# Kernel optimization log

Measured on AMD Instinct MI355X. Metric: run time of the kernel, lower is better.

## Reference

```python
import jax, jax.numpy as jnp
import numpy as np

FEAT_DIM = 128
MAX_ATOMS = 15
MAX_AA = 22
MAX_RELPOS = 32
NUM_FUNCS = 3
BB_N, BB_CA, BB_C = 0, 1, 2  # backbone heavy-atom indices


def setup_inputs() -> dict:
    key = jax.random.key(0)
    ks = jax.random.split(key, 12)
    N, L, A, D = 2, 256, MAX_ATOMS, FEAT_DIM
    s = 0.02
    aa = jax.random.randint(ks[0], (N, L), 0, MAX_AA)
    res_nb = jnp.sort(jax.random.randint(ks[1], (N, L), 0, 500), axis=1)
    chain_nb = jax.random.randint(ks[2], (N, L), 0, 2)
    pos_atoms = jax.random.normal(ks[3], (N, L, A, 3), dtype=jnp.float32) * 3.0
    mask_atoms = jnp.ones((N, L, A), dtype=jnp.float32)
    dihed_dim = 2 * (1 + 4 * NUM_FUNCS)  # 26
    return dict(
        aa=aa, res_nb=res_nb, chain_nb=chain_nb,
        pos_atoms=pos_atoms, mask_atoms=mask_atoms,
        aa_embed_w=jax.random.normal(ks[4], (MAX_AA * MAX_AA, D), jnp.float32) * s,
        relpos_embed_w=jax.random.normal(ks[5], (2 * MAX_RELPOS + 1, D), jnp.float32) * s,
        distcoef_w=jnp.zeros((MAX_AA * MAX_AA, A * A), jnp.float32),  # Constant(0.0) init
        dist_w1=jax.random.normal(ks[6], (A * A, D), jnp.float32) * s,
        dist_b1=jnp.zeros((D,), jnp.float32),
        dist_w2=jax.random.normal(ks[7], (D, D), jnp.float32) * s,
        dist_b2=jnp.zeros((D,), jnp.float32),
        out_w1=jax.random.normal(ks[8], (3 * D + dihed_dim, D), jnp.float32) * s,
        out_b1=jnp.zeros((D,), jnp.float32),
        out_w2=jax.random.normal(ks[9], (D, D), jnp.float32) * s,
        out_b2=jnp.zeros((D,), jnp.float32),
        out_w3=jax.random.normal(ks[10], (D, D), jnp.float32) * s,
        out_b3=jnp.zeros((D,), jnp.float32),
    )


def _dihedral(p0, p1, p2, p3, eps=1e-10):
    # dihedral angle from four points, broadcasting over leading dims
    v0 = p2 - p1
    v1 = p0 - p1
    v2 = p3 - p2
    u1 = jnp.cross(v0, v1)
    u2 = jnp.cross(v0, v2)
    n1 = u1 / jnp.sqrt(jnp.sum(u1 * u1, -1, keepdims=True) + eps)
    n2 = u2 / jnp.sqrt(jnp.sum(u2 * u2, -1, keepdims=True) + eps)
    sgn = jnp.sign(jnp.sum(jnp.cross(v0, n1) * n2, -1))
    cosang = jnp.clip(jnp.sum(n1 * n2, -1), -1.0 + 1e-7, 1.0 - 1e-7)
    return jnp.nan_to_num(sgn * jnp.arccos(cosang))


def _angular_encoding(x):
    # freq bands [1,2,3, 1,1/2,1/3] (num_funcs=3); out dim = d*(1+4*num_funcs)
    freqs = jnp.asarray([1.0, 2.0, 3.0, 1.0, 0.5, 1.0 / 3.0], dtype=x.dtype)
    xe = x[..., None]
    code = jnp.concatenate([xe, jnp.sin(xe * freqs), jnp.cos(xe * freqs)], axis=-1)
    return code.reshape(x.shape[:-1] + (-1,))


def reference(aa, res_nb, chain_nb, pos_atoms, mask_atoms,
              aa_embed_w, relpos_embed_w, distcoef_w,
              dist_w1, dist_b1, dist_w2, dist_b2,
              out_w1, out_b1, out_w2, out_b2, out_w3, out_b3):
    N, L = aa.shape
    A = mask_atoms.shape[-1]

    mask_res = mask_atoms[:, :, BB_CA]                      # (N,L)
    mask_pair = mask_res[:, :, None] * mask_res[:, None, :]  # (N,L,L)

    # amino-acid pair embedding
    aa_pair = aa[:, :, None] * MAX_AA + aa[:, None, :]       # (N,L,L)
    feat_aapair = aa_embed_w[aa_pair]                        # (N,L,L,D)

    # relative position embedding, zeroed across chains
    same_chain = (chain_nb[:, :, None] == chain_nb[:, None, :])
    relpos = jnp.clip(res_nb[:, :, None] - res_nb[:, None, :], -MAX_RELPOS, MAX_RELPOS)
    feat_relpos = relpos_embed_w[relpos + MAX_RELPOS] * same_chain[..., None].astype(pos_atoms.dtype)

    # pairwise atom distances in nm -> gaussian RBF with learned per-aa-pair coef
    diff = pos_atoms[:, :, None, :, None, :] - pos_atoms[:, None, :, None, :, :]  # (N,L,L,A,A,3)
    d = (jnp.sqrt(jnp.sum(diff * diff, axis=-1) + 1e-10) / 10.0).reshape(N, L, L, A * A)
    c = jax.nn.softplus(distcoef_w[aa_pair])                 # (N,L,L,A*A)
    d_gauss = jnp.exp(-c * d * d)
    mask_atom_pair = (mask_atoms[:, :, None, :, None] * mask_atoms[:, None, :, None, :]).reshape(N, L, L, A * A)
    h = jax.nn.relu((d_gauss * mask_atom_pair) @ dist_w1 + dist_b1)
    feat_dist = jax.nn.relu(h @ dist_w2 + dist_b2)           # (N,L,L,D)

    # pairwise dihedrals: inter-residue phi/psi
    pN = pos_atoms[:, :, BB_N]
    pCA = pos_atoms[:, :, BB_CA]
    pC = pos_atoms[:, :, BB_C]
    phi = _dihedral(pC[:, :, None], pN[:, None, :], pCA[:, None, :], pC[:, None, :])
    psi = _dihedral(pN[:, :, None], pCA[:, :, None], pC[:, :, None], pN[:, None, :])
    feat_dihed = _angular_encoding(jnp.stack([phi, psi], axis=-1))  # (N,L,L,26)

    feat_all = jnp.concatenate([feat_aapair, feat_relpos, feat_dist, feat_dihed], axis=-1)
    h = jax.nn.relu(feat_all @ out_w1 + out_b1)
    h = jax.nn.relu(h @ out_w2 + out_b2)
    h = h @ out_w3 + out_b3
    return h * mask_pair[..., None]
```

## Files before the change

kernel.cpp:

```cpp
#include <hip/hip_runtime.h>
#include <math.h>

typedef __attribute__((ext_vector_type(8))) short bf16x8;
typedef __attribute__((ext_vector_type(4))) float f32x4;
typedef unsigned short u16;

#define L_SEQ 256
#define TMP 16
#define MFMA __builtin_amdgcn_mfma_f32_16x16x32_bf16

#define WS_B1   0
#define WS_B2   32768
#define WS_B3   49152
#define WS_B4   102400
#define WS_B5   118784
#define WS_L4LO 135168
#define WS_L5LO 151552
#define WS_TOTAL 167936
#define SP_N    108900

__device__ inline u16 f2bf(float f){
    unsigned u = __float_as_uint(f);
    unsigned r = (u + 0x7FFFu + ((u >> 16) & 1u)) >> 16;
    return (u16)r;
}
__device__ inline float bf2f(u16 h){ return __uint_as_float(((unsigned)h) << 16); }
__device__ inline int swz(int m, int k, int lda){ return m*lda + (k ^ ((m & 7) << 3)); }

struct F3 { float x, y, z; };
__device__ inline F3 f3sub(F3 a, F3 b){ return {a.x-b.x, a.y-b.y, a.z-b.z}; }
__device__ inline F3 f3cross(F3 a, F3 b){
    return {a.y*b.z - a.z*b.y, a.z*b.x - a.x*b.z, a.x*b.y - a.y*b.x};
}
__device__ inline float f3dot(F3 a, F3 b){ return a.x*b.x + a.y*b.y + a.z*b.z; }

__device__ inline float dihedral(F3 p0, F3 p1, F3 p2, F3 p3){
    F3 v0 = f3sub(p2, p1);
    F3 v1 = f3sub(p0, p1);
    F3 v2 = f3sub(p3, p2);
    F3 u1 = f3cross(v0, v1);
    F3 u2 = f3cross(v0, v2);
    float in1 = rsqrtf(f3dot(u1, u1) + 1e-10f);
    float in2 = rsqrtf(f3dot(u2, u2) + 1e-10f);
    F3 n1 = {u1.x*in1, u1.y*in1, u1.z*in1};
    F3 n2 = {u2.x*in2, u2.y*in2, u2.z*in2};
    float s = f3dot(f3cross(v0, n1), n2);
    float sgn = (s > 0.f) ? 1.f : ((s < 0.f) ? -1.f : 0.f);
    float c = f3dot(n1, n2);
    c = fminf(fmaxf(c, -1.f + 1e-7f), 1.f - 1e-7f);
    return sgn * acosf(c);
}

__global__ __launch_bounds__(256)
void prep_w(const float* __restrict__ w1, const float* __restrict__ w2,
            const float* __restrict__ w3, const float* __restrict__ w4,
            const float* __restrict__ w5, u16* __restrict__ ws)
{
    int idx = blockIdx.x * 256 + threadIdx.x;
    if (idx >= WS_TOTAL) return;
    const float* W; int Kreal, rel; bool lo = false;
    if      (idx < WS_B2)   { W = w1; Kreal = 225; rel = idx; }
    else if (idx < WS_B3)   { W = w2; Kreal = 128; rel = idx - WS_B2; }
    else if (idx < WS_B4)   { W = w3; Kreal = 410; rel = idx - WS_B3; }
    else if (idx < WS_B5)   { W = w4; Kreal = 128; rel = idx - WS_B4; }
    else if (idx < WS_L4LO) { W = w5; Kreal = 128; rel = idx - WS_B5; }
    else if (idx < WS_L5LO) { W = w4; Kreal = 128; rel = idx - WS_L4LO; lo = true; }
    else                    { W = w5; Kreal = 128; rel = idx - WS_L5LO; lo = true; }
    int e = rel & 7, lane = (rel >> 3) & 63, ct = (rel >> 9) & 7, kt = rel >> 12;
    int k = kt*32 + ((lane >> 4) << 3) + e;
    int col = ct*16 + (lane & 15);
    float v = (k < Kreal) ? W[k*128 + col] : 0.f;
    u16 h = f2bf(v);
    ws[idx] = lo ? f2bf(v - bf2f(h)) : h;
}

__global__ __launch_bounds__(256)
void prep_sp(const float* __restrict__ dc, float* __restrict__ sp)
{
    int i = blockIdx.x * 256 + threadIdx.x;
    if (i < SP_N){
        float cw = dc[i];
        sp[i] = fmaxf(cw, 0.f) + log1pf(expf(-fabsf(cw)));
    }
}

template<int T>
__device__ inline void gemm16d(const u16* __restrict__ A0, const u16* __restrict__ A1,
                               int lda, const u16* __restrict__ B,
                               int ct, int lane, f32x4 acc[2])
{
    const int r15 = lane & 15;
    const int koff = (lane >> 4) << 3;
    const int sx = (r15 & 7) << 3;
    const u16* a0p = A0 + r15*lda;
    const u16* a1p = A1 + r15*lda;
#pragma unroll
    for (int kt = 0; kt < T; ++kt){
        int kk = ((kt << 5) + koff) ^ sx;
        bf16x8 a0 = *(const bf16x8*)(a0p + kk);
        bf16x8 a1 = *(const bf16x8*)(a1p + kk);
        bf16x8 b  = *(const bf16x8*)(B + (((kt*8 + ct)*64 + lane) << 3));
        acc[0] = MFMA(a0, b, acc[0], 0, 0, 0);
        acc[1] = MFMA(a1, b, acc[1], 0, 0, 0);
    }
}

template<int T>
__device__ inline void gemm16ds(const u16* __restrict__ Ah0, const u16* __restrict__ Al0,
                                const u16* __restrict__ Ah1, const u16* __restrict__ Al1,
                                int lda, const u16* __restrict__ Bh, const u16* __restrict__ Bl,
                                int ct, int lane, f32x4 acc[2])
{
    const int r15 = lane & 15;
    const int koff = (lane >> 4) << 3;
    const int sx = (r15 & 7) << 3;
#pragma unroll
    for (int kt = 0; kt < T; ++kt){
        int kk = ((kt << 5) + koff) ^ sx;
        bf16x8 ah0 = *(const bf16x8*)(Ah0 + r15*lda + kk);
        bf16x8 al0 = *(const bf16x8*)(Al0 + r15*lda + kk);
        bf16x8 ah1 = *(const bf16x8*)(Ah1 + r15*lda + kk);
        bf16x8 al1 = *(const bf16x8*)(Al1 + r15*lda + kk);
        const int bo = ((kt*8 + ct)*64 + lane) << 3;
        bf16x8 bh = *(const bf16x8*)(Bh + bo);
        bf16x8 bl = *(const bf16x8*)(Bl + bo);
        acc[0] = MFMA(ah0, bh, acc[0], 0, 0, 0);
        acc[0] = MFMA(ah0, bl, acc[0], 0, 0, 0);
        acc[0] = MFMA(al0, bh, acc[0], 0, 0, 0);
        acc[1] = MFMA(ah1, bh, acc[1], 0, 0, 0);
        acc[1] = MFMA(ah1, bl, acc[1], 0, 0, 0);
        acc[1] = MFMA(al1, bh, acc[1], 0, 0, 0);
    }
}

__device__ inline void epi16d(f32x4 acc[2], const float* __restrict__ bias,
                              int ct, int lane,
                              u16* D0hi, u16* D0lo, u16* D1hi, u16* D1lo)
{
    const int rr = (lane >> 4) << 2;
    const int col = ct*16 + (lane & 15);
    const float b = bias[col];
#pragma unroll
    for (int r = 0; r < 4; ++r){
        int m = rr + r;
        int idx = m*128 + (col ^ ((m & 7) << 3));
        float v0 = fmaxf(acc[0][r] + b, 0.f);
        float v1 = fmaxf(acc[1][r] + b, 0.f);
        u16 h0 = f2bf(v0), h1 = f2bf(v1);
        D0hi[idx] = h0;
        D1hi[idx] = h1;
        if (D0lo) D0lo[idx] = f2bf(v0 - bf2f(h0));
        if (D1lo) D1lo[idx] = f2bf(v1 - bf2f(h1));
    }
}

__global__ __launch_bounds__(512, 6)
void rpe_mfma5(const int* __restrict__ aa, const int* __restrict__ res_nb,
               const int* __restrict__ chain_nb,
               const float* __restrict__ pos_atoms, const float* __restrict__ mask_atoms,
               const float* __restrict__ aa_embed_w, const float* __restrict__ relpos_embed_w,
               const float* __restrict__ sp_table,
               const float* __restrict__ dist_b1, const float* __restrict__ dist_b2,
               const float* __restrict__ out_b1, const float* __restrict__ out_b2,
               const float* __restrict__ out_b3,
               const u16* __restrict__ ws, float* __restrict__ out)
{
    const int t  = threadIdx.x;
    const int g  = t >> 8;
    const int tl = t & 255;
    const int bid = blockIdx.x;
    const int n  = bid >> 11;
    const int i  = (bid >> 3) & 255;
    const int j0b = (bid & 7) << 5;
    const int j0 = j0b + g*16;
    const int ri = n*L_SEQ + i;
    const int rj0 = n*L_SEQ + j0;

    __shared__ __align__(16) u16 s_g[2][TMP*256];
    __shared__ __align__(16) u16 s_c1[2][TMP*256];
    __shared__ __align__(16) u16 s_c2[2][TMP*128];
    __shared__ __align__(16) u16 s_c3[2][TMP*64];
    __shared__ __align__(16) u16 s_h1s[2][TMP*128];
    __shared__ int   s_aap[2][TMP];
    __shared__ int   s_rp[2][TMP];
    __shared__ float s_same[2][TMP];
    __shared__ float s_mpair[2][TMP];

    float* stage   = (float*)s_h1s[g];
    float* u_posj  = stage;
    float* u_posi  = stage + 720;
    float* u_maskj = stage + 768;
    float* u_maski = stage + 1008;

    for (int idx = tl; idx < TMP*45; idx += 256) u_posj[idx] = pos_atoms[rj0*45 + idx];
    if (tl < 45) u_posi[tl] = pos_atoms[ri*45 + tl];
    for (int idx = tl; idx < TMP*15; idx += 256) u_maskj[idx] = mask_atoms[rj0*15 + idx];
    if (tl >= 64 && tl < 79) u_maski[tl - 64] = mask_atoms[ri*15 + (tl - 64)];
    if (tl >= 96 && tl < 96 + TMP){
        int m = tl - 96, rj = rj0 + m;
        s_aap[g][m] = aa[ri]*22 + aa[rj];
        int d = res_nb[ri] - res_nb[rj];
        d = min(max(d, -32), 32);
        s_rp[g][m] = d + 32;
        s_same[g][m] = (chain_nb[ri] == chain_nb[rj]) ? 1.f : 0.f;
    }
    __syncthreads();

    if (tl < TMP) s_mpair[g][tl] = u_maski[1] * u_maskj[tl*15 + 1];

    {
        const int kg = tl;
        const bool act = kg < 225;
        int ga = 0, gb = 0;
        float pix = 0, piy = 0, piz = 0, mi_a = 0;
        if (act){
            ga = kg / 15; gb = kg - ga*15;
            pix = u_posi[ga*3+0]; piy = u_posi[ga*3+1]; piz = u_posi[ga*3+2];
            mi_a = u_maski[ga];
        }
#pragma unroll 4
        for (int m = 0; m < TMP; ++m){
            float gv = 0.f;
            if (act){
                float dx = pix - u_posj[m*45 + gb*3+0];
                float dy = piy - u_posj[m*45 + gb*3+1];
                float dz = piz - u_posj[m*45 + gb*3+2];
                float d2 = (dx*dx + dy*dy + dz*dz + 1e-10f) * 0.01f;
                float c = sp_table[s_aap[g][m]*225 + kg];
                gv = expf(-c*d2) * mi_a * u_maskj[m*15 + gb];
            }
            s_g[g][swz(m, kg, 256)] = f2bf(gv);
        }
    }

    {
        const int c = tl & 127;
        const int mb = tl >> 7;
#pragma unroll
        for (int it = 0; it < 8; ++it){
            int m = mb + it*2;
            s_c1[g][swz(m, c,       256)] = f2bf(aa_embed_w[s_aap[g][m]*128 + c]);
            s_c1[g][swz(m, 128 + c, 256)] = f2bf(s_same[g][m] * relpos_embed_w[s_rp[g][m]*128 + c]);
        }
    }

    if (tl < 2*TMP){
        int m = tl >> 1, w = tl & 1;
        F3 P0, P1, P2, P3;
        if (w == 0){
            P0 = {u_posi[6],  u_posi[7],  u_posi[8]};
            P1 = {u_posj[m*45+0], u_posj[m*45+1], u_posj[m*45+2]};
            P2 = {u_posj[m*45+3], u_posj[m*45+4], u_posj[m*45+5]};
            P3 = {u_posj[m*45+6], u_posj[m*45+7], u_posj[m*45+8]};
        } else {
            P0 = {u_posi[0], u_posi[1], u_posi[2]};
            P1 = {u_posi[3], u_posi[4], u_posi[5]};
            P2 = {u_posi[6], u_posi[7], u_posi[8]};
            P3 = {u_posj[m*45+0], u_posj[m*45+1], u_posj[m*45+2]};
        }
        float x = dihedral(P0, P1, P2, P3);
        int kb = w*13;
        u16* c3 = s_c3[g];
        c3[swz(m, kb+0,  64)] = f2bf(x);
        c3[swz(m, kb+1,  64)] = f2bf(sinf(x));
        c3[swz(m, kb+2,  64)] = f2bf(sinf(2.f*x));
        c3[swz(m, kb+3,  64)] = f2bf(sinf(3.f*x));
        c3[swz(m, kb+4,  64)] = f2bf(sinf(x));
        c3[swz(m, kb+5,  64)] = f2bf(sinf(0.5f*x));
        c3[swz(m, kb+6,  64)] = f2bf(sinf(x*(1.f/3.f)));
        c3[swz(m, kb+7,  64)] = f2bf(cosf(x));
        c3[swz(m, kb+8,  64)] = f2bf(cosf(2.f*x));
        c3[swz(m, kb+9,  64)] = f2bf(cosf(3.f*x));
        c3[swz(m, kb+10, 64)] = f2bf(cosf(x));
        c3[swz(m, kb+11, 64)] = f2bf(cosf(0.5f*x));
        c3[swz(m, kb+12, 64)] = f2bf(cosf(x*(1.f/3.f)));
    }
    for (int idx = tl; idx < TMP*38; idx += 256){ int m = idx/38; s_c3[g][swz(m, 26 + idx - m*38, 64)] = 0; }
    __syncthreads();

    const int lane = t & 63;
    const int w = t >> 6;

    u16* h3h0 = s_g[0];   u16* h3l0 = s_g[0]  + 2048;
    u16* h3h1 = s_g[1];   u16* h3l1 = s_g[1]  + 2048;
    u16* h4h0 = s_c1[0];  u16* h4l0 = s_c1[0] + 2048;
    u16* h4h1 = s_c1[1];  u16* h4l1 = s_c1[1] + 2048;

    f32x4 acc[2];
    acc[0] = {0,0,0,0}; acc[1] = {0,0,0,0};
    gemm16d<8>(s_g[0], s_g[1], 256, ws + WS_B1, w, lane, acc);
    epi16d(acc, dist_b1, w, lane, s_h1s[0], nullptr, s_h1s[1], nullptr);
    __syncthreads();

    acc[0] = {0,0,0,0}; acc[1] = {0,0,0,0};
    gemm16d<4>(s_h1s[0], s_h1s[1], 128, ws + WS_B2, w, lane, acc);
    epi16d(acc, dist_b2, w, lane, s_c2[0], nullptr, s_c2[1], nullptr);
    __syncthreads();

    acc[0] = {0,0,0,0}; acc[1] = {0,0,0,0};
    gemm16d<8>(s_c1[0], s_c1[1], 256, ws + WS_B3,           w, lane, acc);
    gemm16d<4>(s_c2[0], s_c2[1], 128, ws + WS_B3 +  8*4096, w, lane, acc);
    gemm16d<1>(s_c3[0], s_c3[1],  64, ws + WS_B3 + 12*4096, w, lane, acc);
    epi16d(acc, out_b1, w, lane, h3h0, h3l0, h3h1, h3l1);
    __syncthreads();

    acc[0] = {0,0,0,0}; acc[1] = {0,0,0,0};
    gemm16ds<4>(h3h0, h3l0, h3h1, h3l1, 128, ws + WS_B4, ws + WS_L4LO, w, lane, acc);
    epi16d(acc, out_b2, w, lane, h4h0, h4l0, h4h1, h4l1);
    __syncthreads();

    acc[0] = {0,0,0,0}; acc[1] = {0,0,0,0};
    gemm16ds<4>(h4h0, h4l0, h4h1, h4l1, 128, ws + WS_B5, ws + WS_L5LO, w, lane, acc);
    {
        const int rr = (lane >> 4) << 2;
        const int col = w*16 + (lane & 15);
        const float b = out_b3[col];
#pragma unroll
        for (int gg = 0; gg < 2; ++gg){
            int jg = j0b + gg*16;
#pragma unroll
            for (int r = 0; r < 4; ++r){
                int m = rr + r;
                out[((size_t)(ri*L_SEQ) + (size_t)(jg + m))*128 + col] = (acc[gg][r] + b) * s_mpair[gg][m];
            }
        }
    }
}

extern "C" void kernel_launch(void* const* d_in, const int* in_sizes, int n_in,
                              void* d_out, int out_size, void* d_ws, size_t ws_size,
                              hipStream_t stream) {
    const int*   aa             = (const int*)  d_in[0];
    const int*   res_nb         = (const int*)  d_in[1];
    const int*   chain_nb       = (const int*)  d_in[2];
    const float* pos_atoms      = (const float*)d_in[3];
    const float* mask_atoms     = (const float*)d_in[4];
    const float* aa_embed_w     = (const float*)d_in[5];
    const float* relpos_embed_w = (const float*)d_in[6];
    const float* distcoef_w     = (const float*)d_in[7];
    const float* dist_w1        = (const float*)d_in[8];
    const float* dist_b1        = (const float*)d_in[9];
    const float* dist_w2        = (const float*)d_in[10];
    const float* dist_b2        = (const float*)d_in[11];
    const float* out_w1         = (const float*)d_in[12];
    const float* out_b1         = (const float*)d_in[13];
    const float* out_w2         = (const float*)d_in[14];
    const float* out_b2         = (const float*)d_in[15];
    const float* out_w3         = (const float*)d_in[16];
    const float* out_b3         = (const float*)d_in[17];
    float* out = (float*)d_out;
    u16* ws = (u16*)d_ws;
    float* sp = (float*)(ws + WS_TOTAL);

    hipLaunchKernelGGL(prep_w, dim3((WS_TOTAL + 255)/256), dim3(256), 0, stream,
                       dist_w1, dist_w2, out_w1, out_w2, out_w3, ws);
    hipLaunchKernelGGL(prep_sp, dim3((SP_N + 255)/256), dim3(256), 0, stream,
                       distcoef_w, sp);

    const int nblocks = 2 * L_SEQ * (L_SEQ / 32);
    hipLaunchKernelGGL(rpe_mfma5, dim3(nblocks), dim3(512), 0, stream,
                       aa, res_nb, chain_nb, pos_atoms, mask_atoms,
                       aa_embed_w, relpos_embed_w, sp,
                       dist_b1, dist_b2, out_b1, out_b2, out_b3,
                       ws, out);
}
```

Before: 120.2 us.

## Pre-convert embedding tables to bf16 and gather with padded vector loads

```diff
diff --git a/kernel.cpp b/kernel.cpp
--- a/kernel.cpp
+++ b/kernel.cpp
@@ -18,6 +18,10 @@
 #define WS_L5LO 151552
 #define WS_TOTAL 167936
 #define SP_N    108900
+#define WS_EA   385736
+#define WS_ER   447688
+#define NE_A    61952
+#define NE_R    8448
 
 __device__ inline u16 f2bf(float f){
     unsigned u = __float_as_uint(f);
@@ -25,7 +29,6 @@
     return (u16)r;
 }
 __device__ inline float bf2f(u16 h){ return __uint_as_float(((unsigned)h) << 16); }
-__device__ inline int swz(int m, int k, int lda){ return m*lda + (k ^ ((m & 7) << 3)); }
 
 struct F3 { float x, y, z; };
 __device__ inline F3 f3sub(F3 a, F3 b){ return {a.x-b.x, a.y-b.y, a.z-b.z}; }
@@ -75,23 +78,27 @@
 }
 
 __global__ __launch_bounds__(256)
-void prep_sp(const float* __restrict__ dc, float* __restrict__ sp)
+void prep_t(const float* __restrict__ dc, const float* __restrict__ aaw,
+            const float* __restrict__ rpw, u16* __restrict__ ws)
 {
     int i = blockIdx.x * 256 + threadIdx.x;
+    float* sp = (float*)(ws + WS_TOTAL);
     if (i < SP_N){
         float cw = dc[i];
-        sp[i] = fmaxf(cw, 0.f) + log1pf(expf(-fabsf(cw)));
-    }
-}
-
-template<int T>
+        sp[i] = (fmaxf(cw, 0.f) + log1pf(expf(-fabsf(cw)))) * 0.01f;
+    }
+    if (i < NE_A) ws[WS_EA + i] = f2bf(aaw[i]);
+    if (i < NE_R) ws[WS_ER + i] = (i >> 7) < 65 ? f2bf(rpw[i]) : (u16)0;
+}
+
+template<int T, bool SWZ>
 __device__ inline void gemm16d(const u16* __restrict__ A0, const u16* __restrict__ A1,
                                int lda, const u16* __restrict__ B,
                                int ct, int lane, f32x4 acc[2])
 {
     const int r15 = lane & 15;
     const int koff = (lane >> 4) << 3;
-    const int sx = (r15 & 7) << 3;
+    const int sx = SWZ ? ((r15 & 7) << 3) : 0;
     const u16* a0p = A0 + r15*lda;
     const u16* a1p = A1 + r15*lda;
 #pragma unroll
@@ -155,11 +162,9 @@
 }
 
 __global__ __launch_bounds__(512, 6)
-void rpe_mfma5(const int* __restrict__ aa, const int* __restrict__ res_nb,
+void rpe_mfma6(const int* __restrict__ aa, const int* __restrict__ res_nb,
                const int* __restrict__ chain_nb,
                const float* __restrict__ pos_atoms, const float* __restrict__ mask_atoms,
-               const float* __restrict__ aa_embed_w, const float* __restrict__ relpos_embed_w,
-               const float* __restrict__ sp_table,
                const float* __restrict__ dist_b1, const float* __restrict__ dist_b2,
                const float* __restrict__ out_b1, const float* __restrict__ out_b2,
                const float* __restrict__ out_b3,
@@ -176,15 +181,17 @@
     const int ri = n*L_SEQ + i;
     const int rj0 = n*L_SEQ + j0;
 
-    __shared__ __align__(16) u16 s_g[2][TMP*256];
-    __shared__ __align__(16) u16 s_c1[2][TMP*256];
+    __shared__ __align__(16) u16 s_g[2][TMP*264];
+    __shared__ __align__(16) u16 s_c1[2][TMP*264];
     __shared__ __align__(16) u16 s_c2[2][TMP*128];
-    __shared__ __align__(16) u16 s_c3[2][TMP*64];
+    __shared__ __align__(16) u16 s_c3[2][TMP*32];
     __shared__ __align__(16) u16 s_h1s[2][TMP*128];
-    __shared__ int   s_aap[2][TMP];
-    __shared__ int   s_rp[2][TMP];
-    __shared__ float s_same[2][TMP];
+    __shared__ int   s_aapE[2][TMP];
+    __shared__ int   s_aapS[2][TMP];
+    __shared__ int   s_rpE[2][TMP];
     __shared__ float s_mpair[2][TMP];
+
+    const float* sp_table = (const float*)(ws + WS_TOTAL);
 
     float* stage   = (float*)s_h1s[g];
     float* u_posj  = stage;
@@ -198,11 +205,13 @@
     if (tl >= 64 && tl < 79) u_maski[tl - 64] = mask_atoms[ri*15 + (tl - 64)];
     if (tl >= 96 && tl < 96 + TMP){
         int m = tl - 96, rj = rj0 + m;
-        s_aap[g][m] = aa[ri]*22 + aa[rj];
+        int aap = aa[ri]*22 + aa[rj];
+        s_aapE[g][m] = aap << 8;
+        s_aapS[g][m] = aap * 225;
         int d = res_nb[ri] - res_nb[rj];
         d = min(max(d, -32), 32);
-        s_rp[g][m] = d + 32;
-        s_same[g][m] = (chain_nb[ri] == chain_nb[rj]) ? 1.f : 0.f;
+        bool same = (chain_nb[ri] == chain_nb[rj]);
+        s_rpE[g][m] = (same ? (d + 32) : 65) << 8;
     }
     __syncthreads();
 
@@ -211,36 +220,37 @@
     {
         const int kg = tl;
         const bool act = kg < 225;
-        int ga = 0, gb = 0;
-        float pix = 0, piy = 0, piz = 0, mi_a = 0;
         if (act){
-            ga = kg / 15; gb = kg - ga*15;
-            pix = u_posi[ga*3+0]; piy = u_posi[ga*3+1]; piz = u_posi[ga*3+2];
-            mi_a = u_maski[ga];
-        }
-#pragma unroll 4
-        for (int m = 0; m < TMP; ++m){
-            float gv = 0.f;
-            if (act){
+            int ga = kg / 15, gb = kg - ga*15;
+            float pix = u_posi[ga*3+0], piy = u_posi[ga*3+1], piz = u_posi[ga*3+2];
+            float mi_a = u_maski[ga];
+#pragma unroll
+            for (int m = 0; m < TMP; ++m){
                 float dx = pix - u_posj[m*45 + gb*3+0];
                 float dy = piy - u_posj[m*45 + gb*3+1];
                 float dz = piz - u_posj[m*45 + gb*3+2];
-                float d2 = (dx*dx + dy*dy + dz*dz + 1e-10f) * 0.01f;
-                float c = sp_table[s_aap[g][m]*225 + kg];
-                gv = expf(-c*d2) * mi_a * u_maskj[m*15 + gb];
+                float d2 = fmaf(dz, dz, fmaf(dy, dy, fmaf(dx, dx, 1e-10f)));
+                float c  = sp_table[s_aapS[g][m] + kg];
+                float gv = expf(-c*d2) * (mi_a * u_maskj[m*15 + gb]);
+                s_g[g][m*264 + kg] = f2bf(gv);
             }
-            s_g[g][swz(m, kg, 256)] = f2bf(gv);
+        } else {
+#pragma unroll
+            for (int m = 0; m < TMP; ++m) s_g[g][m*264 + kg] = 0;
         }
     }
 
     {
-        const int c = tl & 127;
-        const int mb = tl >> 7;
-#pragma unroll
-        for (int it = 0; it < 8; ++it){
-            int m = mb + it*2;
-            s_c1[g][swz(m, c,       256)] = f2bf(aa_embed_w[s_aap[g][m]*128 + c]);
-            s_c1[g][swz(m, 128 + c, 256)] = f2bf(s_same[g][m] * relpos_embed_w[s_rp[g][m]*128 + c]);
+        const u16* EA = ws + WS_EA;
+        const u16* ER = ws + WS_ER;
+#pragma unroll
+        for (int it = 0; it < 2; ++it){
+            int cid = tl + it*256;
+            int m = cid >> 5, ch = cid & 31;
+            const u16* src = (ch < 16)
+                ? (const u16*)((const char*)EA + s_aapE[g][m] + (ch << 4))
+                : (const u16*)((const char*)ER + s_rpE[g][m] + ((ch - 16) << 4));
+            *(bf16x8*)(s_c1[g] + m*264 + (ch << 3)) = *(const bf16x8*)src;
         }
     }
 
@@ -259,23 +269,22 @@
             P3 = {u_posj[m*45+0], u_posj[m*45+1], u_posj[m*45+2]};
         }
         float x = dihedral(P0, P1, P2, P3);
-        int kb = w*13;
-        u16* c3 = s_c3[g];
-        c3[swz(m, kb+0,  64)] = f2bf(x);
-        c3[swz(m, kb+1,  64)] = f2bf(sinf(x));
-        c3[swz(m, kb+2,  64)] = f2bf(sinf(2.f*x));
-        c3[swz(m, kb+3,  64)] = f2bf(sinf(3.f*x));
-        c3[swz(m, kb+4,  64)] = f2bf(sinf(x));
-        c3[swz(m, kb+5,  64)] = f2bf(sinf(0.5f*x));
-        c3[swz(m, kb+6,  64)] = f2bf(sinf(x*(1.f/3.f)));
-        c3[swz(m, kb+7,  64)] = f2bf(cosf(x));
-        c3[swz(m, kb+8,  64)] = f2bf(cosf(2.f*x));
-        c3[swz(m, kb+9,  64)] = f2bf(cosf(3.f*x));
-        c3[swz(m, kb+10, 64)] = f2bf(cosf(x));
-        c3[swz(m, kb+11, 64)] = f2bf(cosf(0.5f*x));
-        c3[swz(m, kb+12, 64)] = f2bf(cosf(x*(1.f/3.f)));
-    }
-    for (int idx = tl; idx < TMP*38; idx += 256){ int m = idx/38; s_c3[g][swz(m, 26 + idx - m*38, 64)] = 0; }
+        u16* c3 = s_c3[g] + m*32 + w*13;
+        c3[0]  = f2bf(x);
+        c3[1]  = f2bf(sinf(x));
+        c3[2]  = f2bf(sinf(2.f*x));
+        c3[3]  = f2bf(sinf(3.f*x));
+        c3[4]  = f2bf(sinf(x));
+        c3[5]  = f2bf(sinf(0.5f*x));
+        c3[6]  = f2bf(sinf(x*(1.f/3.f)));
+        c3[7]  = f2bf(cosf(x));
+        c3[8]  = f2bf(cosf(2.f*x));
+        c3[9]  = f2bf(cosf(3.f*x));
+        c3[10] = f2bf(cosf(x));
+        c3[11] = f2bf(cosf(0.5f*x));
+        c3[12] = f2bf(cosf(x*(1.f/3.f)));
+    }
+    if (tl < TMP*6){ int m = tl/6; s_c3[g][m*32 + 26 + tl - m*6] = 0; }
     __syncthreads();
 
     const int lane = t & 63;
@@ -288,19 +297,19 @@
 
     f32x4 acc[2];
     acc[0] = {0,0,0,0}; acc[1] = {0,0,0,0};
-    gemm16d<8>(s_g[0], s_g[1], 256, ws + WS_B1, w, lane, acc);
+    gemm16d<8,false>(s_g[0], s_g[1], 264, ws + WS_B1, w, lane, acc);
     epi16d(acc, dist_b1, w, lane, s_h1s[0], nullptr, s_h1s[1], nullptr);
     __syncthreads();
 
     acc[0] = {0,0,0,0}; acc[1] = {0,0,0,0};
-    gemm16d<4>(s_h1s[0], s_h1s[1], 128, ws + WS_B2, w, lane, acc);
+    gemm16d<4,true>(s_h1s[0], s_h1s[1], 128, ws + WS_B2, w, lane, acc);
     epi16d(acc, dist_b2, w, lane, s_c2[0], nullptr, s_c2[1], nullptr);
     __syncthreads();
 
     acc[0] = {0,0,0,0}; acc[1] = {0,0,0,0};
-    gemm16d<8>(s_c1[0], s_c1[1], 256, ws + WS_B3,           w, lane, acc);
-    gemm16d<4>(s_c2[0], s_c2[1], 128, ws + WS_B3 +  8*4096, w, lane, acc);
-    gemm16d<1>(s_c3[0], s_c3[1],  64, ws + WS_B3 + 12*4096, w, lane, acc);
+    gemm16d<8,false>(s_c1[0], s_c1[1], 264, ws + WS_B3,           w, lane, acc);
+    gemm16d<4,true >(s_c2[0], s_c2[1], 128, ws + WS_B3 +  8*4096, w, lane, acc);
+    gemm16d<1,false>(s_c3[0], s_c3[1],  32, ws + WS_B3 + 12*4096, w, lane, acc);
     epi16d(acc, out_b1, w, lane, h3h0, h3l0, h3h1, h3l1);
     __syncthreads();
 
@@ -350,17 +359,15 @@
     const float* out_b3         = (const float*)d_in[17];
     float* out = (float*)d_out;
     u16* ws = (u16*)d_ws;
-    float* sp = (float*)(ws + WS_TOTAL);
 
     hipLaunchKernelGGL(prep_w, dim3((WS_TOTAL + 255)/256), dim3(256), 0, stream,
                        dist_w1, dist_w2, out_w1, out_w2, out_w3, ws);
-    hipLaunchKernelGGL(prep_sp, dim3((SP_N + 255)/256), dim3(256), 0, stream,
-                       distcoef_w, sp);
+    hipLaunchKernelGGL(prep_t, dim3((SP_N + 255)/256), dim3(256), 0, stream,
+                       distcoef_w, aa_embed_w, relpos_embed_w, ws);
 
     const int nblocks = 2 * L_SEQ * (L_SEQ / 32);
-    hipLaunchKernelGGL(rpe_mfma5, dim3(nblocks), dim3(512), 0, stream,
+    hipLaunchKernelGGL(rpe_mfma6, dim3(nblocks), dim3(512), 0, stream,
                        aa, res_nb, chain_nb, pos_atoms, mask_atoms,
-                       aa_embed_w, relpos_embed_w, sp,
                        dist_b1, dist_b2, out_b1, out_b2, out_b3,
                        ws, out);
 }
```

New measurement: 108.5 us. 9.7% less time.
